# Performance work log

Hardware: AMD Instinct MI355X
Metric: run time of the kernel (lower is better)

The kernel has to match this reference:

```python
import jax, jax.numpy as jnp
import numpy as np

N_QUBITS = 10
N_LAYERS = 2
BATCH = 8192
N_PARAMS = 5 * N_QUBITS * N_LAYERS  # 100
C64 = jnp.complex64

# ---- batched 2x2 gate matrices (theta: (B,)) ----

def _rx(theta):
    h = theta * 0.5
    c = jnp.cos(h).astype(C64)
    s = (-1j * jnp.sin(h).astype(C64))
    return jnp.stack([jnp.stack([c, s], -1), jnp.stack([s, c], -1)], -2)

def _ry(theta):
    h = theta * 0.5
    c = jnp.cos(h).astype(C64)
    s = jnp.sin(h).astype(C64)
    return jnp.stack([jnp.stack([c, -s], -1), jnp.stack([s, c], -1)], -2)

def _rz(theta):
    h = theta.astype(jnp.float32) * 0.5
    e0 = jnp.exp(-1j * h.astype(C64))
    e1 = jnp.exp(1j * h.astype(C64))
    z = jnp.zeros_like(e0)
    return jnp.stack([jnp.stack([e0, z], -1), jnp.stack([z, e1], -1)], -2)

# psi layout: (B, 2, 2, ..., 2); axis 1+w corresponds to wire w (PennyLane order: wire 0 = MSB)

def _apply_1q(psi, mat, w):
    psi = jnp.moveaxis(psi, 1 + w, -1)
    sh = psi.shape
    out = jnp.einsum('bij,bkj->bki', mat, psi.reshape(sh[0], -1, 2))
    return jnp.moveaxis(out.reshape(sh), -1, 1 + w)

def _apply_crx(psi, theta, ctrl, tgt):
    psi = jnp.moveaxis(psi, [1 + ctrl, 1 + tgt], [-2, -1])
    sh = psi.shape
    p = psi.reshape(sh[0], -1, 2, 2)  # axes: (batch, rest, ctrl, tgt)
    h = theta * 0.5
    c = jnp.cos(h)[:, None].astype(C64)
    s = (-1j * jnp.sin(h)[:, None].astype(C64))
    a0 = p[..., 1, 0]
    a1 = p[..., 1, 1]
    p1 = jnp.stack([c * a0 + s * a1, s * a0 + c * a1], -1)
    p = jnp.stack([p[..., 0, :], p1], -2)
    return jnp.moveaxis(p.reshape(sh), [-2, -1], [1 + ctrl, 1 + tgt])

def _init_state(angles):
    B = angles.shape[0]
    psi = jnp.zeros((B, 2 ** N_QUBITS), C64).at[:, 0].set(1.0)
    psi = psi.reshape((B,) + (2,) * N_QUBITS)
    for i in range(N_QUBITS):  # RY input embedding
        psi = _apply_1q(psi, _ry(angles[:, i]), i)
    return psi

def _delta_layer(psi, params, dt, off):
    for i in range(N_QUBITS):
        psi = _apply_1q(psi, _rx(params[:, off] * dt), i)
        psi = _apply_1q(psi, _ry(params[:, off + 1] * dt), i)
        psi = _apply_1q(psi, _rz(params[:, off + 2] * dt), i)
        off += 3
    for i in range(N_QUBITS):
        psi = _apply_crx(psi, params[:, off], i, (i + 1) % N_QUBITS); off += 1
    for i in range(N_QUBITS - 1, -1, -1):
        psi = _apply_crx(psi, params[:, off], i, (i - 1) % N_QUBITS); off += 1
    return psi, off

def _backward_layer(psi, params, dt, off):
    for i in range(N_QUBITS - 1, -1, -1):
        psi = _apply_1q(psi, _rx(params[:, off] * dt), i)
        psi = _apply_1q(psi, _ry(params[:, off + 1] * dt), i)
        psi = _apply_1q(psi, _rz(params[:, off + 2] * dt), i)
        off += 3
    for i in range(N_QUBITS - 1, -1, -1):
        psi = _apply_crx(psi, params[:, off], i, (i - 1) % N_QUBITS); off += 1
    for i in range(N_QUBITS):
        psi = _apply_crx(psi, params[:, off], i, (i + 1) % N_QUBITS); off += 1
    return psi, off

def _unified_layer(psi, params, off):
    for i in range(N_QUBITS):
        psi = _apply_1q(psi, _rx(params[:, off]), i)
        psi = _apply_1q(psi, _ry(params[:, off + 1]), i)
        psi = _apply_1q(psi, _rz(params[:, off + 2]), i)
        off += 3
    for i in range(N_QUBITS):
        psi = _apply_crx(psi, params[:, off], i, (i + 1) % N_QUBITS); off += 1
    for i in range(N_QUBITS - 1, -1, -1):
        psi = _apply_crx(psi, params[:, off], i, (i - 1) % N_QUBITS); off += 1
    return psi, off

def _forward_circuit(angles, params, dt):
    psi = _init_state(angles); off = 0
    for _ in range(N_LAYERS):
        psi, off = _delta_layer(psi, params, dt, off)
    return psi.reshape(psi.shape[0], -1)

def _backward_circuit(angles, params, dt):
    psi = _init_state(angles); off = 0
    for _ in range(N_LAYERS):
        psi, off = _backward_layer(psi, params, dt, off)
    return psi.reshape(psi.shape[0], -1)

def _diagonal_circuit(angles, params):
    psi = _init_state(angles); off = 0
    for _ in range(N_LAYERS):
        psi, off = _unified_layer(psi, params, off)
    return psi.reshape(psi.shape[0], -1)

def _measure(psi_flat):
    # Pauli X/Y/Z expectations per qubit -> (B, 3*n_qubits), ordered [X..., Y..., Z...]
    B = psi_flat.shape[0]
    t = psi_flat.reshape((B,) + (2,) * N_QUBITS)
    Xs, Ys, Zs = [], [], []
    for w in range(N_QUBITS):
        p = jnp.moveaxis(t, 1 + w, -1).reshape(B, -1, 2)
        cross = jnp.sum(jnp.conj(p[..., 0]) * p[..., 1], axis=1)
        Xs.append(2.0 * cross.real)
        Ys.append(2.0 * cross.imag)
        Zs.append(jnp.sum(jnp.abs(p[..., 0]) ** 2 - jnp.abs(p[..., 1]) ** 2, axis=1))
    return jnp.stack(Xs + Ys + Zs, axis=1)

def setup_inputs() -> dict:
    key = jax.random.key(0)
    k1, k2, k3, k4, k5 = jax.random.split(key, 5)
    init_val = np.float32(1.0 / np.sqrt(3.0))
    return {
        'input_angles': jax.random.normal(k1, (BATCH, N_QUBITS), jnp.float32),
        'forward_params': jax.random.normal(k2, (BATCH, N_PARAMS), jnp.float32),
        'backward_params': jax.random.normal(k3, (BATCH, N_PARAMS), jnp.float32),
        'diagonal_params': jax.random.normal(k4, (BATCH, N_PARAMS), jnp.float32),
        'dt_scale': jax.random.uniform(k5, (BATCH,), jnp.float32),
        'alpha_real': jnp.asarray(init_val), 'alpha_imag': jnp.asarray(0.0, jnp.float32),
        'beta_real': jnp.asarray(init_val), 'beta_imag': jnp.asarray(0.0, jnp.float32),
        'gamma_real': jnp.asarray(init_val), 'gamma_imag': jnp.asarray(0.0, jnp.float32),
    }

def reference(input_angles, forward_params, backward_params, diagonal_params, dt_scale,
              alpha_real, alpha_imag, beta_real, beta_imag, gamma_real, gamma_imag):
    psi1 = _forward_circuit(input_angles, forward_params, dt_scale)
    psi2 = _backward_circuit(input_angles, backward_params, dt_scale)
    psi3 = _diagonal_circuit(input_angles, diagonal_params)
    alpha = jax.lax.complex(alpha_real, alpha_imag).astype(C64)
    beta = jax.lax.complex(beta_real, beta_imag).astype(C64)
    gamma = jax.lax.complex(gamma_real, gamma_imag).astype(C64)
    norm = jnp.sqrt(jnp.abs(alpha) ** 2 + jnp.abs(beta) ** 2 + jnp.abs(gamma) ** 2 + 1e-9).astype(C64)
    psi = (alpha / norm) * psi1 + (beta / norm) * psi2 + (gamma / norm) * psi3
    vnorm = jnp.linalg.norm(psi, axis=-1, keepdims=True) + 1e-9
    psi = psi / vnorm.astype(C64)
    return _measure(psi).astype(jnp.float32)
```

## Files before the change

### kernel.cpp

```cpp
#include <hip/hip_runtime.h>

#define NQ    10
#define NPRM  100
#define NBATCH 8192

using F2 = __attribute__((ext_vector_type(2))) float;

__device__ __forceinline__ F2 mk2(float a, float b) { F2 v; v.x = a; v.y = b; return v; }


template<int LM>
__device__ __forceinline__ float lshf(float v) {
  if constexpr (LM == 1) {
    int r = __builtin_amdgcn_update_dpp(0, __builtin_bit_cast(int, v), 0xB1, 0xF, 0xF, true);
    return __builtin_bit_cast(float, r);
  } else if constexpr (LM == 2) {
    int r = __builtin_amdgcn_update_dpp(0, __builtin_bit_cast(int, v), 0x4E, 0xF, 0xF, true);
    return __builtin_bit_cast(float, r);
  } else if constexpr (LM == 8) {
    int r = __builtin_amdgcn_update_dpp(0, __builtin_bit_cast(int, v), 0x128, 0xF, 0xF, true);
    return __builtin_bit_cast(float, r);
  } else {
    return __shfl_xor(v, LM, 64);
  }
}
template<int LM>
__device__ __forceinline__ F2 lshf2(F2 v) {
  return mk2(lshf<LM>(v.x), lshf<LM>(v.y));
}



template<int P>
__device__ __forceinline__ void g_rx(F2* st, unsigned lane, float c, float s) {
  if constexpr (P < 4) {
    constexpr int m = 1 << P;
#pragma unroll
    for (int r = 0; r < 16; ++r) if (!(r & m)) {
      const int r1 = r | m;
      F2 a0 = st[r], a1 = st[r1];
      st[r]  = mk2(c*a0.x + s*a1.y, c*a0.y - s*a1.x);
      st[r1] = mk2(s*a0.y + c*a1.x, c*a1.y - s*a0.x);
    }
  } else {
    constexpr int lm = 1 << (P - 4);
#pragma unroll
    for (int r = 0; r < 16; ++r) {
      float mx = st[r].x, my = st[r].y;
      float ox = lshf<lm>(mx), oy = lshf<lm>(my);
      st[r] = mk2(c*mx + s*oy, c*my - s*ox);
    }
  }
}

template<int P>
__device__ __forceinline__ void g_u(F2* st, unsigned lane, F2 u00, F2 u01) {
  if constexpr (P < 4) {
    constexpr int m = 1 << P;
#pragma unroll
    for (int r = 0; r < 16; ++r) if (!(r & m)) {
      const int r1 = r | m;
      F2 a0 = st[r], a1 = st[r1];
      st[r]  = mk2(u00.x*a0.x - u00.y*a0.y + u01.x*a1.x - u01.y*a1.y,
                   u00.x*a0.y + u00.y*a0.x + u01.x*a1.y + u01.y*a1.x);
      st[r1] = mk2(-u01.x*a0.x - u01.y*a0.y + u00.x*a1.x + u00.y*a1.y,
                   -u01.x*a0.y + u01.y*a0.x + u00.x*a1.y - u00.y*a1.x);
    }
  } else {
    constexpr int lm = 1 << (P - 4);
    const bool hi = (lane & lm) != 0;
    const float vax = u00.x,               vay = hi ? -u00.y : u00.y;
    const float vbx = hi ? -u01.x : u01.x, vby = u01.y;
#pragma unroll
    for (int r = 0; r < 16; ++r) {
      float mx = st[r].x, my = st[r].y;
      float ox = lshf<lm>(mx), oy = lshf<lm>(my);
      st[r] = mk2(vax*mx - vay*my + vbx*ox - vby*oy,
                  vax*my + vay*mx + vbx*oy + vby*ox);
    }
  }
}

template<int TB, int CB>
__device__ __forceinline__ void g_crx(F2* st, unsigned lane, float c, float s) {
  if constexpr (CB >= 4) {
    const bool act = (lane >> (CB - 4)) & 1u;
    const float ce = act ? c : 1.0f;
    const float se = act ? s : 0.0f;
    g_rx<TB>(st, lane, ce, se);
  } else {
    constexpr int cm = 1 << CB;
    if constexpr (TB < 4) {
#pragma unroll
      for (int r = 0; r < 16; ++r) if ((r & cm) && !(r & (1 << TB))) {
        const int r1 = r | (1 << TB);
        F2 a0 = st[r], a1 = st[r1];
        st[r]  = mk2(c*a0.x + s*a1.y, c*a0.y - s*a1.x);
        st[r1] = mk2(s*a0.y + c*a1.x, c*a1.y - s*a0.x);
      }
    } else {
      constexpr int lm = 1 << (TB - 4);
#pragma unroll
      for (int r = 0; r < 16; ++r) if (r & cm) {
        float mx = st[r].x, my = st[r].y;
        float ox = lshf<lm>(mx), oy = lshf<lm>(my);
        st[r] = mk2(c*mx + s*oy, c*my - s*ox);
      }
    }
  }
}

__device__ __forceinline__ void g_u_w(F2* st, unsigned lane, int w, F2 u00, F2 u01) {
  switch (w) {
    case 0: g_u<9>(st,lane,u00,u01); break;
    case 1: g_u<8>(st,lane,u00,u01); break;
    case 2: g_u<7>(st,lane,u00,u01); break;
    case 3: g_u<6>(st,lane,u00,u01); break;
    case 4: g_u<5>(st,lane,u00,u01); break;
    case 5: g_u<4>(st,lane,u00,u01); break;
    case 6: g_u<3>(st,lane,u00,u01); break;
    case 7: g_u<2>(st,lane,u00,u01); break;
    case 8: g_u<1>(st,lane,u00,u01); break;
    case 9: g_u<0>(st,lane,u00,u01); break;
  }
}

#define CRX_CASE(CW,TW) case (CW)*10+(TW): g_crx<9-(TW), 9-(CW)>(st,lane,c,s); break;
__device__ __forceinline__ void crx_w(F2* st, unsigned lane, int cw, int tw, float c, float s) {
  switch (cw * 10 + tw) {
    CRX_CASE(0,1) CRX_CASE(1,2) CRX_CASE(2,3) CRX_CASE(3,4) CRX_CASE(4,5)
    CRX_CASE(5,6) CRX_CASE(6,7) CRX_CASE(7,8) CRX_CASE(8,9) CRX_CASE(9,0)
    CRX_CASE(1,0) CRX_CASE(2,1) CRX_CASE(3,2) CRX_CASE(4,3) CRX_CASE(5,4)
    CRX_CASE(6,5) CRX_CASE(7,6) CRX_CASE(8,7) CRX_CASE(9,8) CRX_CASE(0,9)
  }
}

__device__ __forceinline__ void make_u(float ax, float ay, float az, F2& u00, F2& u01) {
  float ca, sa, cb, sb, cg, sg;
  __sincosf(ax*0.5f, &sa, &ca);
  __sincosf(ay*0.5f, &sb, &cb);
  __sincosf(az*0.5f, &sg, &cg);
  const float m00x =  cb*ca, m00y =  sb*sa;
  const float m01x = -sb*ca, m01y = -cb*sa;
  u00 = mk2(m00x*cg + m00y*sg, m00y*cg - m00x*sg);
  u01 = mk2(m01x*cg + m01y*sg, m01y*cg - m01x*sg);
}

__device__ __forceinline__ void layer_bwd(F2* st, unsigned lane, const float* P, float dt, int& off) {
#pragma unroll
  for (int i = NQ-1; i >= 0; --i) {
    F2 u00, u01;
    make_u(P[off]*dt, P[off+1]*dt, P[off+2]*dt, u00, u01);
    g_u_w(st, lane, i, u00, u01);
    off += 3;
  }
#pragma unroll
  for (int i = NQ-1; i >= 0; --i) {
    float s, c; __sincosf(P[off]*0.5f, &s, &c);
    crx_w(st, lane, i, (i+NQ-1)%NQ, c, s); ++off;
  }
#pragma unroll
  for (int i = 0; i < NQ; ++i) {
    float s, c; __sincosf(P[off]*0.5f, &s, &c);
    crx_w(st, lane, i, (i+1)%NQ, c, s); ++off;
  }
}

__device__ __forceinline__ void init_state(F2* st, unsigned lane, const float* ang) {
  float cw[NQ], sw[NQ];
#pragma unroll
  for (int w = 0; w < NQ; ++w) __sincosf(ang[w]*0.5f, &sw[w], &cw[w]);
  float L = 1.0f;
#pragma unroll
  for (int q = 0; q < 6; ++q)
    L *= ((lane >> q) & 1u) ? sw[5-q] : cw[5-q];
#pragma unroll
  for (int r = 0; r < 16; ++r) {
    float R = L;
#pragma unroll
    for (int p = 0; p < 4; ++p)
      R *= ((r >> p) & 1) ? sw[9-p] : cw[9-p];
    st[r] = mk2(R, 0.0f);
  }
}


struct UU { F2 x00, y00, x01, y01; };

template<int P>
__device__ __forceinline__ void g_u2(F2* sR, F2* sI, unsigned lane, UU u) {
  if constexpr (P < 4) {
    constexpr int m = 1 << P;
#pragma unroll
    for (int r = 0; r < 16; ++r) if (!(r & m)) {
      const int r1 = r | m;
      F2 R0 = sR[r], I0 = sI[r], R1 = sR[r1], I1 = sI[r1];
      sR[r]  = u.x00*R0 - u.y00*I0 + u.x01*R1 - u.y01*I1;
      sI[r]  = u.x00*I0 + u.y00*R0 + u.x01*I1 + u.y01*R1;
      sR[r1] = u.x00*R1 + u.y00*I1 - u.x01*R0 - u.y01*I0;
      sI[r1] = u.x00*I1 - u.y00*R1 - u.x01*I0 + u.y01*R0;
    }
  } else {
    constexpr int lm = 1 << (P - 4);
    const bool hi = (lane & lm) != 0;
    const F2 vay = mk2(hi ? -u.y00.x : u.y00.x, hi ? -u.y00.y : u.y00.y);
    const F2 vbx = mk2(hi ? -u.x01.x : u.x01.x, hi ? -u.x01.y : u.x01.y);
#pragma unroll
    for (int r = 0; r < 16; ++r) {
      F2 R = sR[r], I = sI[r];
      F2 oR = lshf2<lm>(R), oI = lshf2<lm>(I);
      sR[r] = u.x00*R - vay*I + vbx*oR - u.y01*oI;
      sI[r] = u.x00*I + vay*R + vbx*oI + u.y01*oR;
    }
  }
}

template<int P>
__device__ __forceinline__ void g_rx2(F2* sR, F2* sI, unsigned lane, F2 C, F2 S) {
  if constexpr (P < 4) {
    constexpr int m = 1 << P;
#pragma unroll
    for (int r = 0; r < 16; ++r) if (!(r & m)) {
      const int r1 = r | m;
      F2 R0 = sR[r], I0 = sI[r], R1 = sR[r1], I1 = sI[r1];
      sR[r]  = C*R0 + S*I1;
      sI[r]  = C*I0 - S*R1;
      sR[r1] = C*R1 + S*I0;
      sI[r1] = C*I1 - S*R0;
    }
  } else {
    constexpr int lm = 1 << (P - 4);
#pragma unroll
    for (int r = 0; r < 16; ++r) {
      F2 R = sR[r], I = sI[r];
      F2 oR = lshf2<lm>(R), oI = lshf2<lm>(I);
      sR[r] = C*R + S*oI;
      sI[r] = C*I - S*oR;
    }
  }
}

template<int TB, int CB>
__device__ __forceinline__ void g_crx2(F2* sR, F2* sI, unsigned lane, F2 C, F2 S) {
  if constexpr (CB >= 4) {
    const bool act = (lane >> (CB - 4)) & 1u;
    const F2 Ce = mk2(act ? C.x : 1.0f, act ? C.y : 1.0f);
    const F2 Se = mk2(act ? S.x : 0.0f, act ? S.y : 0.0f);
    g_rx2<TB>(sR, sI, lane, Ce, Se);
  } else {
    constexpr int cm = 1 << CB;
    if constexpr (TB < 4) {
#pragma unroll
      for (int r = 0; r < 16; ++r) if ((r & cm) && !(r & (1 << TB))) {
        const int r1 = r | (1 << TB);
        F2 R0 = sR[r], I0 = sI[r], R1 = sR[r1], I1 = sI[r1];
        sR[r]  = C*R0 + S*I1;
        sI[r]  = C*I0 - S*R1;
        sR[r1] = C*R1 + S*I0;
        sI[r1] = C*I1 - S*R0;
      }
    } else {
      constexpr int lm = 1 << (TB - 4);
#pragma unroll
      for (int r = 0; r < 16; ++r) if (r & cm) {
        F2 R = sR[r], I = sI[r];
        F2 oR = lshf2<lm>(R), oI = lshf2<lm>(I);
        sR[r] = C*R + S*oI;
        sI[r] = C*I - S*oR;
      }
    }
  }
}

__device__ __forceinline__ void g_u2_w(F2* sR, F2* sI, unsigned lane, int w, UU u) {
  switch (w) {
    case 0: g_u2<9>(sR,sI,lane,u); break;
    case 1: g_u2<8>(sR,sI,lane,u); break;
    case 2: g_u2<7>(sR,sI,lane,u); break;
    case 3: g_u2<6>(sR,sI,lane,u); break;
    case 4: g_u2<5>(sR,sI,lane,u); break;
    case 5: g_u2<4>(sR,sI,lane,u); break;
    case 6: g_u2<3>(sR,sI,lane,u); break;
    case 7: g_u2<2>(sR,sI,lane,u); break;
    case 8: g_u2<1>(sR,sI,lane,u); break;
    case 9: g_u2<0>(sR,sI,lane,u); break;
  }
}

#define CRX2_CASE(CW,TW) case (CW)*10+(TW): g_crx2<9-(TW), 9-(CW)>(sR,sI,lane,C,S); break;
__device__ __forceinline__ void crx2_w(F2* sR, F2* sI, unsigned lane, int cw, int tw, F2 C, F2 S) {
  switch (cw * 10 + tw) {
    CRX2_CASE(0,1) CRX2_CASE(1,2) CRX2_CASE(2,3) CRX2_CASE(3,4) CRX2_CASE(4,5)
    CRX2_CASE(5,6) CRX2_CASE(6,7) CRX2_CASE(7,8) CRX2_CASE(8,9) CRX2_CASE(9,0)
    CRX2_CASE(1,0) CRX2_CASE(2,1) CRX2_CASE(3,2) CRX2_CASE(4,3) CRX2_CASE(5,4)
    CRX2_CASE(6,5) CRX2_CASE(7,6) CRX2_CASE(8,7) CRX2_CASE(9,8) CRX2_CASE(0,9)
  }
}

__device__ __forceinline__ void layer_fwd2(F2* sR, F2* sI, unsigned lane,
                                           const float* Pf, const float* Pd, float dt, int& off) {
#pragma unroll
  for (int i = 0; i < NQ; ++i) {
    F2 u00F, u01F, u00D, u01D;
    make_u(Pf[off]*dt, Pf[off+1]*dt, Pf[off+2]*dt, u00F, u01F);
    make_u(Pd[off],    Pd[off+1],    Pd[off+2],    u00D, u01D);
    UU u;
    u.x00 = mk2(u00F.x, u00D.x); u.y00 = mk2(u00F.y, u00D.y);
    u.x01 = mk2(u01F.x, u01D.x); u.y01 = mk2(u01F.y, u01D.y);
    g_u2_w(sR, sI, lane, i, u);
    off += 3;
  }
#pragma unroll
  for (int i = 0; i < NQ; ++i) {
    float sF, cF, sD, cD;
    __sincosf(Pf[off]*0.5f, &sF, &cF);
    __sincosf(Pd[off]*0.5f, &sD, &cD);
    crx2_w(sR, sI, lane, i, (i+1)%NQ, mk2(cF,cD), mk2(sF,sD)); ++off;
  }
#pragma unroll
  for (int i = NQ-1; i >= 0; --i) {
    float sF, cF, sD, cD;
    __sincosf(Pf[off]*0.5f, &sF, &cF);
    __sincosf(Pd[off]*0.5f, &sD, &cD);
    crx2_w(sR, sI, lane, i, (i+NQ-1)%NQ, mk2(cF,cD), mk2(sF,sD)); ++off;
  }
}

__device__ __forceinline__ void init_state2(F2* sR, F2* sI, unsigned lane, const float* ang) {
  float cw[NQ], sw[NQ];
#pragma unroll
  for (int w = 0; w < NQ; ++w) __sincosf(ang[w]*0.5f, &sw[w], &cw[w]);
  float L = 1.0f;
#pragma unroll
  for (int q = 0; q < 6; ++q)
    L *= ((lane >> q) & 1u) ? sw[5-q] : cw[5-q];
#pragma unroll
  for (int r = 0; r < 16; ++r) {
    float R = L;
#pragma unroll
    for (int p = 0; p < 4; ++p)
      R *= ((r >> p) & 1) ? sw[9-p] : cw[9-p];
    sR[r] = mk2(R, R);
    sI[r] = mk2(0.0f, 0.0f);
  }
}


template<int P>
__device__ __forceinline__ void meas(const F2* st, unsigned lane, float& X, float& Y, float& Z) {
  float cr = 0.f, ci = 0.f, z = 0.f;
  if constexpr (P < 4) {
    constexpr int m = 1 << P;
#pragma unroll
    for (int r = 0; r < 16; ++r) if (!(r & m)) {
      const int r1 = r | m;
      F2 a0 = st[r], a1 = st[r1];
      cr += a0.x*a1.x + a0.y*a1.y;
      ci += a0.x*a1.y - a0.y*a1.x;
      z  += (a0.x*a0.x + a0.y*a0.y) - (a1.x*a1.x + a1.y*a1.y);
    }
    cr *= 2.f; ci *= 2.f;
  } else {
    constexpr int lm = 1 << (P - 4);
    const bool hi = (lane & lm) != 0;
#pragma unroll
    for (int r = 0; r < 16; ++r) {
      float mx = st[r].x, my = st[r].y;
      float ox = lshf<lm>(mx), oy = lshf<lm>(my);
      float a0x = hi ? ox : mx, a0y = hi ? oy : my;
      float a1x = hi ? mx : ox, a1y = hi ? my : oy;
      cr += a0x*a1x + a0y*a1y;
      ci += a0x*a1y - a0y*a1x;
      float p2 = mx*mx + my*my;
      z += hi ? -p2 : p2;
    }
  }
  X = cr; Y = ci; Z = z;
}

__device__ __forceinline__ float wred(float v) {
  v += lshf<1>(v);
  v += lshf<2>(v);
  v += lshf<4>(v);
  v += lshf<8>(v);
  v += lshf<16>(v);
  v += lshf<32>(v);
  return v;
}


__global__ void __launch_bounds__(256) qsim_kernel(
    const float* __restrict__ angles, const float* __restrict__ fwdP,
    const float* __restrict__ bwdP,   const float* __restrict__ diagP,
    const float* __restrict__ dts,
    const float* __restrict__ ar, const float* __restrict__ ai,
    const float* __restrict__ br, const float* __restrict__ bi,
    const float* __restrict__ gr, const float* __restrict__ gi,
    float* __restrict__ out)
{
  const int tid = blockIdx.x * blockDim.x + threadIdx.x;
  const int b = tid >> 6;
  if (b >= NBATCH) return;
  const unsigned lane = threadIdx.x & 63u;
  const int bu = __builtin_amdgcn_readfirstlane(b);

  const float* ang = angles + bu * NQ;
  const float dt = dts[bu];

  const float arv = ar[0], aiv = ai[0], brv = br[0], biv = bi[0], grv = gr[0], giv = gi[0];
  const float nrm = sqrtf(arv*arv + aiv*aiv + brv*brv + biv*biv + grv*grv + giv*giv + 1e-9f);
  const F2 cA = mk2(arv/nrm, aiv/nrm), cB = mk2(brv/nrm, biv/nrm), cG = mk2(grv/nrm, giv/nrm);

  F2 sR[16], sI[16];
  init_state2(sR, sI, lane, ang);
  { int off = 0;
    const float* Pf = fwdP  + bu*NPRM;
    const float* Pd = diagP + bu*NPRM;
#pragma unroll
    for (int l = 0; l < 2; ++l) layer_fwd2(sR, sI, lane, Pf, Pd, dt, off); }

  F2 stc[16];
#pragma unroll
  for (int r = 0; r < 16; ++r) {
    stc[r] = mk2(cA.x*sR[r].x - cA.y*sI[r].x + cG.x*sR[r].y - cG.y*sI[r].y,
                 cA.x*sI[r].x + cA.y*sR[r].x + cG.x*sI[r].y + cG.y*sR[r].y);
  }

  F2 st[16];
  init_state(st, lane, ang);
  { int off = 0; const float* P = bwdP + bu*NPRM;
#pragma unroll
    for (int l = 0; l < 2; ++l) layer_bwd(st, lane, P, dt, off); }
#pragma unroll
  for (int r = 0; r < 16; ++r) {
    stc[r] = mk2(stc[r].x + cB.x*st[r].x - cB.y*st[r].y,
                 stc[r].y + cB.x*st[r].y + cB.y*st[r].x);
  }

  float n2 = 0.f;
#pragma unroll
  for (int r = 0; r < 16; ++r) n2 += stc[r].x*stc[r].x + stc[r].y*stc[r].y;
  n2 = wred(n2);
  const float inv = 1.0f / (sqrtf(n2) + 1e-9f);
#pragma unroll
  for (int r = 0; r < 16; ++r) { stc[r] = mk2(stc[r].x*inv, stc[r].y*inv); }

  float* o = out + b * 30;
#pragma unroll
  for (int w = 0; w < NQ; ++w) {
    float X, Y, Z;
    switch (w) {
      case 0: meas<9>(stc, lane, X, Y, Z); break;
      case 1: meas<8>(stc, lane, X, Y, Z); break;
      case 2: meas<7>(stc, lane, X, Y, Z); break;
      case 3: meas<6>(stc, lane, X, Y, Z); break;
      case 4: meas<5>(stc, lane, X, Y, Z); break;
      case 5: meas<4>(stc, lane, X, Y, Z); break;
      case 6: meas<3>(stc, lane, X, Y, Z); break;
      case 7: meas<2>(stc, lane, X, Y, Z); break;
      case 8: meas<1>(stc, lane, X, Y, Z); break;
      default: meas<0>(stc, lane, X, Y, Z); break;
    }
    X = wred(X); Y = wred(Y); Z = wred(Z);
    if (lane == 0) { o[w] = X; o[10 + w] = Y; o[20 + w] = Z; }
  }
}

extern "C" void kernel_launch(void* const* d_in, const int* in_sizes, int n_in,
                              void* d_out, int out_size, void* d_ws, size_t ws_size,
                              hipStream_t stream) {
  const float* angles = (const float*)d_in[0];
  const float* fwdP   = (const float*)d_in[1];
  const float* bwdP   = (const float*)d_in[2];
  const float* diagP  = (const float*)d_in[3];
  const float* dts    = (const float*)d_in[4];
  const float* ar     = (const float*)d_in[5];
  const float* ai     = (const float*)d_in[6];
  const float* br     = (const float*)d_in[7];
  const float* bi     = (const float*)d_in[8];
  const float* gr     = (const float*)d_in[9];
  const float* gi     = (const float*)d_in[10];
  float* out = (float*)d_out;

  const int threads = 256;
  const int blocks  = NBATCH / (threads / 64);
  qsim_kernel<<<blocks, threads, 0, stream>>>(
      angles, fwdP, bwdP, diagP, dts, ar, ai, br, bi, gr, gi, out);
}
```

Baseline: 289.2 us.

## Split three circuits across waves, pack two batch items per wave

```diff
diff --git a/kernel.cpp b/kernel.cpp
--- a/kernel.cpp
+++ b/kernel.cpp
@@ -29,160 +29,6 @@
   return mk2(lshf<LM>(v.x), lshf<LM>(v.y));
 }
 
-
-
-template<int P>
-__device__ __forceinline__ void g_rx(F2* st, unsigned lane, float c, float s) {
-  if constexpr (P < 4) {
-    constexpr int m = 1 << P;
-#pragma unroll
-    for (int r = 0; r < 16; ++r) if (!(r & m)) {
-      const int r1 = r | m;
-      F2 a0 = st[r], a1 = st[r1];
-      st[r]  = mk2(c*a0.x + s*a1.y, c*a0.y - s*a1.x);
-      st[r1] = mk2(s*a0.y + c*a1.x, c*a1.y - s*a0.x);
-    }
-  } else {
-    constexpr int lm = 1 << (P - 4);
-#pragma unroll
-    for (int r = 0; r < 16; ++r) {
-      float mx = st[r].x, my = st[r].y;
-      float ox = lshf<lm>(mx), oy = lshf<lm>(my);
-      st[r] = mk2(c*mx + s*oy, c*my - s*ox);
-    }
-  }
-}
-
-template<int P>
-__device__ __forceinline__ void g_u(F2* st, unsigned lane, F2 u00, F2 u01) {
-  if constexpr (P < 4) {
-    constexpr int m = 1 << P;
-#pragma unroll
-    for (int r = 0; r < 16; ++r) if (!(r & m)) {
-      const int r1 = r | m;
-      F2 a0 = st[r], a1 = st[r1];
-      st[r]  = mk2(u00.x*a0.x - u00.y*a0.y + u01.x*a1.x - u01.y*a1.y,
-                   u00.x*a0.y + u00.y*a0.x + u01.x*a1.y + u01.y*a1.x);
-      st[r1] = mk2(-u01.x*a0.x - u01.y*a0.y + u00.x*a1.x + u00.y*a1.y,
-                   -u01.x*a0.y + u01.y*a0.x + u00.x*a1.y - u00.y*a1.x);
-    }
-  } else {
-    constexpr int lm = 1 << (P - 4);
-    const bool hi = (lane & lm) != 0;
-    const float vax = u00.x,               vay = hi ? -u00.y : u00.y;
-    const float vbx = hi ? -u01.x : u01.x, vby = u01.y;
-#pragma unroll
-    for (int r = 0; r < 16; ++r) {
-      float mx = st[r].x, my = st[r].y;
-      float ox = lshf<lm>(mx), oy = lshf<lm>(my);
-      st[r] = mk2(vax*mx - vay*my + vbx*ox - vby*oy,
-                  vax*my + vay*mx + vbx*oy + vby*ox);
-    }
-  }
-}
-
-template<int TB, int CB>
-__device__ __forceinline__ void g_crx(F2* st, unsigned lane, float c, float s) {
-  if constexpr (CB >= 4) {
-    const bool act = (lane >> (CB - 4)) & 1u;
-    const float ce = act ? c : 1.0f;
-    const float se = act ? s : 0.0f;
-    g_rx<TB>(st, lane, ce, se);
-  } else {
-    constexpr int cm = 1 << CB;
-    if constexpr (TB < 4) {
-#pragma unroll
-      for (int r = 0; r < 16; ++r) if ((r & cm) && !(r & (1 << TB))) {
-        const int r1 = r | (1 << TB);
-        F2 a0 = st[r], a1 = st[r1];
-        st[r]  = mk2(c*a0.x + s*a1.y, c*a0.y - s*a1.x);
-        st[r1] = mk2(s*a0.y + c*a1.x, c*a1.y - s*a0.x);
-      }
-    } else {
-      constexpr int lm = 1 << (TB - 4);
-#pragma unroll
-      for (int r = 0; r < 16; ++r) if (r & cm) {
-        float mx = st[r].x, my = st[r].y;
-        float ox = lshf<lm>(mx), oy = lshf<lm>(my);
-        st[r] = mk2(c*mx + s*oy, c*my - s*ox);
-      }
-    }
-  }
-}
-
-__device__ __forceinline__ void g_u_w(F2* st, unsigned lane, int w, F2 u00, F2 u01) {
-  switch (w) {
-    case 0: g_u<9>(st,lane,u00,u01); break;
-    case 1: g_u<8>(st,lane,u00,u01); break;
-    case 2: g_u<7>(st,lane,u00,u01); break;
-    case 3: g_u<6>(st,lane,u00,u01); break;
-    case 4: g_u<5>(st,lane,u00,u01); break;
-    case 5: g_u<4>(st,lane,u00,u01); break;
-    case 6: g_u<3>(st,lane,u00,u01); break;
-    case 7: g_u<2>(st,lane,u00,u01); break;
-    case 8: g_u<1>(st,lane,u00,u01); break;
-    case 9: g_u<0>(st,lane,u00,u01); break;
-  }
-}
-
-#define CRX_CASE(CW,TW) case (CW)*10+(TW): g_crx<9-(TW), 9-(CW)>(st,lane,c,s); break;
-__device__ __forceinline__ void crx_w(F2* st, unsigned lane, int cw, int tw, float c, float s) {
-  switch (cw * 10 + tw) {
-    CRX_CASE(0,1) CRX_CASE(1,2) CRX_CASE(2,3) CRX_CASE(3,4) CRX_CASE(4,5)
-    CRX_CASE(5,6) CRX_CASE(6,7) CRX_CASE(7,8) CRX_CASE(8,9) CRX_CASE(9,0)
-    CRX_CASE(1,0) CRX_CASE(2,1) CRX_CASE(3,2) CRX_CASE(4,3) CRX_CASE(5,4)
-    CRX_CASE(6,5) CRX_CASE(7,6) CRX_CASE(8,7) CRX_CASE(9,8) CRX_CASE(0,9)
-  }
-}
-
-__device__ __forceinline__ void make_u(float ax, float ay, float az, F2& u00, F2& u01) {
-  float ca, sa, cb, sb, cg, sg;
-  __sincosf(ax*0.5f, &sa, &ca);
-  __sincosf(ay*0.5f, &sb, &cb);
-  __sincosf(az*0.5f, &sg, &cg);
-  const float m00x =  cb*ca, m00y =  sb*sa;
-  const float m01x = -sb*ca, m01y = -cb*sa;
-  u00 = mk2(m00x*cg + m00y*sg, m00y*cg - m00x*sg);
-  u01 = mk2(m01x*cg + m01y*sg, m01y*cg - m01x*sg);
-}
-
-__device__ __forceinline__ void layer_bwd(F2* st, unsigned lane, const float* P, float dt, int& off) {
-#pragma unroll
-  for (int i = NQ-1; i >= 0; --i) {
-    F2 u00, u01;
-    make_u(P[off]*dt, P[off+1]*dt, P[off+2]*dt, u00, u01);
-    g_u_w(st, lane, i, u00, u01);
-    off += 3;
-  }
-#pragma unroll
-  for (int i = NQ-1; i >= 0; --i) {
-    float s, c; __sincosf(P[off]*0.5f, &s, &c);
-    crx_w(st, lane, i, (i+NQ-1)%NQ, c, s); ++off;
-  }
-#pragma unroll
-  for (int i = 0; i < NQ; ++i) {
-    float s, c; __sincosf(P[off]*0.5f, &s, &c);
-    crx_w(st, lane, i, (i+1)%NQ, c, s); ++off;
-  }
-}
-
-__device__ __forceinline__ void init_state(F2* st, unsigned lane, const float* ang) {
-  float cw[NQ], sw[NQ];
-#pragma unroll
-  for (int w = 0; w < NQ; ++w) __sincosf(ang[w]*0.5f, &sw[w], &cw[w]);
-  float L = 1.0f;
-#pragma unroll
-  for (int q = 0; q < 6; ++q)
-    L *= ((lane >> q) & 1u) ? sw[5-q] : cw[5-q];
-#pragma unroll
-  for (int r = 0; r < 16; ++r) {
-    float R = L;
-#pragma unroll
-    for (int p = 0; p < 4; ++p)
-      R *= ((r >> p) & 1) ? sw[9-p] : cw[9-p];
-    st[r] = mk2(R, 0.0f);
-  }
-}
 
 
 struct UU { F2 x00, y00, x01, y01; };
@@ -297,99 +143,147 @@
   }
 }
 
+__device__ __forceinline__ void make_u(float ax, float ay, float az, F2& u00, F2& u01) {
+  float ca, sa, cb, sb, cg, sg;
+  __sincosf(ax*0.5f, &sa, &ca);
+  __sincosf(ay*0.5f, &sb, &cb);
+  __sincosf(az*0.5f, &sg, &cg);
+  const float m00x =  cb*ca, m00y =  sb*sa;
+  const float m01x = -sb*ca, m01y = -cb*sa;
+  u00 = mk2(m00x*cg + m00y*sg, m00y*cg - m00x*sg);
+  u01 = mk2(m01x*cg + m01y*sg, m01y*cg - m01x*sg);
+}
+
+__device__ __forceinline__ UU pack_u(const float* P0, const float* P1, float dt0, float dt1, int off) {
+  F2 u00a, u01a, u00b, u01b;
+  make_u(P0[off]*dt0, P0[off+1]*dt0, P0[off+2]*dt0, u00a, u01a);
+  make_u(P1[off]*dt1, P1[off+1]*dt1, P1[off+2]*dt1, u00b, u01b);
+  UU u;
+  u.x00 = mk2(u00a.x, u00b.x); u.y00 = mk2(u00a.y, u00b.y);
+  u.x01 = mk2(u01a.x, u01b.x); u.y01 = mk2(u01a.y, u01b.y);
+  return u;
+}
+
+__device__ __forceinline__ void pack_cs(const float* P0, const float* P1, int off, F2& C, F2& S) {
+  float s0, c0, s1, c1;
+  __sincosf(P0[off]*0.5f, &s0, &c0);
+  __sincosf(P1[off]*0.5f, &s1, &c1);
+  C = mk2(c0, c1); S = mk2(s0, s1);
+}
+
 __device__ __forceinline__ void layer_fwd2(F2* sR, F2* sI, unsigned lane,
-                                           const float* Pf, const float* Pd, float dt, int& off) {
+                                           const float* P0, const float* P1,
+                                           float dt0, float dt1, int& off) {
 #pragma unroll
   for (int i = 0; i < NQ; ++i) {
-    F2 u00F, u01F, u00D, u01D;
-    make_u(Pf[off]*dt, Pf[off+1]*dt, Pf[off+2]*dt, u00F, u01F);
-    make_u(Pd[off],    Pd[off+1],    Pd[off+2],    u00D, u01D);
-    UU u;
-    u.x00 = mk2(u00F.x, u00D.x); u.y00 = mk2(u00F.y, u00D.y);
-    u.x01 = mk2(u01F.x, u01D.x); u.y01 = mk2(u01F.y, u01D.y);
-    g_u2_w(sR, sI, lane, i, u);
+    g_u2_w(sR, sI, lane, i, pack_u(P0, P1, dt0, dt1, off));
     off += 3;
   }
 #pragma unroll
   for (int i = 0; i < NQ; ++i) {
-    float sF, cF, sD, cD;
-    __sincosf(Pf[off]*0.5f, &sF, &cF);
-    __sincosf(Pd[off]*0.5f, &sD, &cD);
-    crx2_w(sR, sI, lane, i, (i+1)%NQ, mk2(cF,cD), mk2(sF,sD)); ++off;
+    F2 C, S; pack_cs(P0, P1, off, C, S);
+    crx2_w(sR, sI, lane, i, (i+1)%NQ, C, S); ++off;
   }
 #pragma unroll
   for (int i = NQ-1; i >= 0; --i) {
-    float sF, cF, sD, cD;
-    __sincosf(Pf[off]*0.5f, &sF, &cF);
-    __sincosf(Pd[off]*0.5f, &sD, &cD);
-    crx2_w(sR, sI, lane, i, (i+NQ-1)%NQ, mk2(cF,cD), mk2(sF,sD)); ++off;
-  }
-}
-
-__device__ __forceinline__ void init_state2(F2* sR, F2* sI, unsigned lane, const float* ang) {
-  float cw[NQ], sw[NQ];
-#pragma unroll
-  for (int w = 0; w < NQ; ++w) __sincosf(ang[w]*0.5f, &sw[w], &cw[w]);
-  float L = 1.0f;
-#pragma unroll
-  for (int q = 0; q < 6; ++q)
-    L *= ((lane >> q) & 1u) ? sw[5-q] : cw[5-q];
+    F2 C, S; pack_cs(P0, P1, off, C, S);
+    crx2_w(sR, sI, lane, i, (i+NQ-1)%NQ, C, S); ++off;
+  }
+}
+
+__device__ __forceinline__ void layer_bwd2(F2* sR, F2* sI, unsigned lane,
+                                           const float* P0, const float* P1,
+                                           float dt0, float dt1, int& off) {
+#pragma unroll
+  for (int i = NQ-1; i >= 0; --i) {
+    g_u2_w(sR, sI, lane, i, pack_u(P0, P1, dt0, dt1, off));
+    off += 3;
+  }
+#pragma unroll
+  for (int i = NQ-1; i >= 0; --i) {
+    F2 C, S; pack_cs(P0, P1, off, C, S);
+    crx2_w(sR, sI, lane, i, (i+NQ-1)%NQ, C, S); ++off;
+  }
+#pragma unroll
+  for (int i = 0; i < NQ; ++i) {
+    F2 C, S; pack_cs(P0, P1, off, C, S);
+    crx2_w(sR, sI, lane, i, (i+1)%NQ, C, S); ++off;
+  }
+}
+
+__device__ __forceinline__ void init_state2e(F2* sR, F2* sI, unsigned lane,
+                                             const float* ang0, const float* ang1) {
+  float cw0[NQ], sw0[NQ], cw1[NQ], sw1[NQ];
+#pragma unroll
+  for (int w = 0; w < NQ; ++w) {
+    __sincosf(ang0[w]*0.5f, &sw0[w], &cw0[w]);
+    __sincosf(ang1[w]*0.5f, &sw1[w], &cw1[w]);
+  }
+  F2 L = mk2(1.0f, 1.0f);
+#pragma unroll
+  for (int q = 0; q < 6; ++q) {
+    const int w = 5-q;
+    L *= ((lane >> q) & 1u) ? mk2(sw0[w], sw1[w]) : mk2(cw0[w], cw1[w]);
+  }
 #pragma unroll
   for (int r = 0; r < 16; ++r) {
-    float R = L;
-#pragma unroll
-    for (int p = 0; p < 4; ++p)
-      R *= ((r >> p) & 1) ? sw[9-p] : cw[9-p];
-    sR[r] = mk2(R, R);
+    F2 R = L;
+#pragma unroll
+    for (int p = 0; p < 4; ++p) {
+      const int w = 9-p;
+      R *= ((r >> p) & 1) ? mk2(sw0[w], sw1[w]) : mk2(cw0[w], cw1[w]);
+    }
+    sR[r] = R;
     sI[r] = mk2(0.0f, 0.0f);
   }
 }
 
 
 template<int P>
-__device__ __forceinline__ void meas(const F2* st, unsigned lane, float& X, float& Y, float& Z) {
-  float cr = 0.f, ci = 0.f, z = 0.f;
+__device__ __forceinline__ void meas2(const F2* sRe, const F2* sIm, unsigned lane,
+                                      F2& X, F2& Y, F2& Z) {
+  F2 cr = mk2(0,0), ci = mk2(0,0), z = mk2(0,0);
   if constexpr (P < 4) {
     constexpr int m = 1 << P;
 #pragma unroll
     for (int r = 0; r < 16; ++r) if (!(r & m)) {
       const int r1 = r | m;
-      F2 a0 = st[r], a1 = st[r1];
-      cr += a0.x*a1.x + a0.y*a1.y;
-      ci += a0.x*a1.y - a0.y*a1.x;
-      z  += (a0.x*a0.x + a0.y*a0.y) - (a1.x*a1.x + a1.y*a1.y);
-    }
-    cr *= 2.f; ci *= 2.f;
+      F2 aR = sRe[r], aI = sIm[r], bR = sRe[r1], bI = sIm[r1];
+      cr += aR*bR + aI*bI;
+      ci += aR*bI - aI*bR;
+      z  += (aR*aR + aI*aI) - (bR*bR + bI*bI);
+    }
+    cr = cr + cr; ci = ci + ci;
   } else {
     constexpr int lm = 1 << (P - 4);
     const bool hi = (lane & lm) != 0;
 #pragma unroll
     for (int r = 0; r < 16; ++r) {
-      float mx = st[r].x, my = st[r].y;
-      float ox = lshf<lm>(mx), oy = lshf<lm>(my);
-      float a0x = hi ? ox : mx, a0y = hi ? oy : my;
-      float a1x = hi ? mx : ox, a1y = hi ? my : oy;
-      cr += a0x*a1x + a0y*a1y;
-      ci += a0x*a1y - a0y*a1x;
-      float p2 = mx*mx + my*my;
+      F2 mR = sRe[r], mI = sIm[r];
+      F2 oR = lshf2<lm>(mR), oI = lshf2<lm>(mI);
+      F2 a0R = hi ? oR : mR, a0I = hi ? oI : mI;
+      F2 a1R = hi ? mR : oR, a1I = hi ? mI : oI;
+      cr += a0R*a1R + a0I*a1I;
+      ci += a0R*a1I - a0I*a1R;
+      F2 p2 = mR*mR + mI*mI;
       z += hi ? -p2 : p2;
     }
   }
   X = cr; Y = ci; Z = z;
 }
 
-__device__ __forceinline__ float wred(float v) {
-  v += lshf<1>(v);
-  v += lshf<2>(v);
-  v += lshf<4>(v);
-  v += lshf<8>(v);
-  v += lshf<16>(v);
-  v += lshf<32>(v);
+__device__ __forceinline__ F2 wred2(F2 v) {
+  v += lshf2<1>(v);
+  v += lshf2<2>(v);
+  v += lshf2<4>(v);
+  v += lshf2<8>(v);
+  v += lshf2<16>(v);
+  v += lshf2<32>(v);
   return v;
 }
 
 
-__global__ void __launch_bounds__(256) qsim_kernel(
+__global__ void __launch_bounds__(192, 2) qsim_kernel(
     const float* __restrict__ angles, const float* __restrict__ fwdP,
     const float* __restrict__ bwdP,   const float* __restrict__ diagP,
     const float* __restrict__ dts,
@@ -398,71 +292,96 @@
     const float* __restrict__ gr, const float* __restrict__ gi,
     float* __restrict__ out)
 {
-  const int tid = blockIdx.x * blockDim.x + threadIdx.x;
-  const int b = tid >> 6;
-  if (b >= NBATCH) return;
+  __shared__ F2 ldsR[2][16][64];
+  __shared__ F2 ldsI[2][16][64];
+
+  const int wave = threadIdx.x >> 6;
   const unsigned lane = threadIdx.x & 63u;
-  const int bu = __builtin_amdgcn_readfirstlane(b);
-
-  const float* ang = angles + bu * NQ;
-  const float dt = dts[bu];
+  const int b0 = blockIdx.x * 2;
+  const int b1 = b0 + 1;
+
+  const float* ang0 = angles + b0 * NQ;
+  const float* ang1 = angles + b1 * NQ;
+  const float dt0 = dts[b0], dt1 = dts[b1];
 
   const float arv = ar[0], aiv = ai[0], brv = br[0], biv = bi[0], grv = gr[0], giv = gi[0];
   const float nrm = sqrtf(arv*arv + aiv*aiv + brv*brv + biv*biv + grv*grv + giv*giv + 1e-9f);
-  const F2 cA = mk2(arv/nrm, aiv/nrm), cB = mk2(brv/nrm, biv/nrm), cG = mk2(grv/nrm, giv/nrm);
+  const float cAx = arv/nrm, cAy = aiv/nrm;
+  const float cBx = brv/nrm, cBy = biv/nrm;
+  const float cGx = grv/nrm, cGy = giv/nrm;
 
   F2 sR[16], sI[16];
-  init_state2(sR, sI, lane, ang);
-  { int off = 0;
-    const float* Pf = fwdP  + bu*NPRM;
-    const float* Pd = diagP + bu*NPRM;
-#pragma unroll
-    for (int l = 0; l < 2; ++l) layer_fwd2(sR, sI, lane, Pf, Pd, dt, off); }
-
-  F2 stc[16];
+  init_state2e(sR, sI, lane, ang0, ang1);
+
+  if (wave == 0) {
+    int off = 0;
+    const float* P0 = fwdP + b0*NPRM;
+    const float* P1 = fwdP + b1*NPRM;
+#pragma unroll
+    for (int l = 0; l < 2; ++l) layer_fwd2(sR, sI, lane, P0, P1, dt0, dt1, off);
+  } else if (wave == 1) {
+    int off = 0;
+    const float* P0 = bwdP + b0*NPRM;
+    const float* P1 = bwdP + b1*NPRM;
+#pragma unroll
+    for (int l = 0; l < 2; ++l) layer_bwd2(sR, sI, lane, P0, P1, dt0, dt1, off);
+  } else {
+    int off = 0;
+    const float* P0 = diagP + b0*NPRM;
+    const float* P1 = diagP + b1*NPRM;
+#pragma unroll
+    for (int l = 0; l < 2; ++l) layer_fwd2(sR, sI, lane, P0, P1, 1.0f, 1.0f, off);
+  }
+
+  if (wave != 0) {
+    const float wx = (wave == 1) ? cBx : cGx;
+    const float wy = (wave == 1) ? cBy : cGy;
+#pragma unroll
+    for (int r = 0; r < 16; ++r) {
+      ldsR[wave-1][r][lane] = wx*sR[r] - wy*sI[r];
+      ldsI[wave-1][r][lane] = wx*sI[r] + wy*sR[r];
+    }
+  }
+  __syncthreads();
+  if (wave != 0) return;
+
 #pragma unroll
   for (int r = 0; r < 16; ++r) {
-    stc[r] = mk2(cA.x*sR[r].x - cA.y*sI[r].x + cG.x*sR[r].y - cG.y*sI[r].y,
-                 cA.x*sI[r].x + cA.y*sR[r].x + cG.x*sI[r].y + cG.y*sR[r].y);
-  }
-
-  F2 st[16];
-  init_state(st, lane, ang);
-  { int off = 0; const float* P = bwdP + bu*NPRM;
-#pragma unroll
-    for (int l = 0; l < 2; ++l) layer_bwd(st, lane, P, dt, off); }
-#pragma unroll
-  for (int r = 0; r < 16; ++r) {
-    stc[r] = mk2(stc[r].x + cB.x*st[r].x - cB.y*st[r].y,
-                 stc[r].y + cB.x*st[r].y + cB.y*st[r].x);
-  }
-
-  float n2 = 0.f;
-#pragma unroll
-  for (int r = 0; r < 16; ++r) n2 += stc[r].x*stc[r].x + stc[r].y*stc[r].y;
-  n2 = wred(n2);
-  const float inv = 1.0f / (sqrtf(n2) + 1e-9f);
-#pragma unroll
-  for (int r = 0; r < 16; ++r) { stc[r] = mk2(stc[r].x*inv, stc[r].y*inv); }
-
-  float* o = out + b * 30;
+    F2 nR = cAx*sR[r] - cAy*sI[r] + ldsR[0][r][lane] + ldsR[1][r][lane];
+    F2 nI = cAx*sI[r] + cAy*sR[r] + ldsI[0][r][lane] + ldsI[1][r][lane];
+    sR[r] = nR; sI[r] = nI;
+  }
+
+  F2 n2 = mk2(0.0f, 0.0f);
+#pragma unroll
+  for (int r = 0; r < 16; ++r) n2 += sR[r]*sR[r] + sI[r]*sI[r];
+  n2 = wred2(n2);
+  const F2 inv = mk2(1.0f/(sqrtf(n2.x)+1e-9f), 1.0f/(sqrtf(n2.y)+1e-9f));
+#pragma unroll
+  for (int r = 0; r < 16; ++r) { sR[r] *= inv; sI[r] *= inv; }
+
+  float* o0 = out + b0 * 30;
+  float* o1 = out + b1 * 30;
 #pragma unroll
   for (int w = 0; w < NQ; ++w) {
-    float X, Y, Z;
+    F2 X, Y, Z;
     switch (w) {
-      case 0: meas<9>(stc, lane, X, Y, Z); break;
-      case 1: meas<8>(stc, lane, X, Y, Z); break;
-      case 2: meas<7>(stc, lane, X, Y, Z); break;
-      case 3: meas<6>(stc, lane, X, Y, Z); break;
-      case 4: meas<5>(stc, lane, X, Y, Z); break;
-      case 5: meas<4>(stc, lane, X, Y, Z); break;
-      case 6: meas<3>(stc, lane, X, Y, Z); break;
-      case 7: meas<2>(stc, lane, X, Y, Z); break;
-      case 8: meas<1>(stc, lane, X, Y, Z); break;
-      default: meas<0>(stc, lane, X, Y, Z); break;
-    }
-    X = wred(X); Y = wred(Y); Z = wred(Z);
-    if (lane == 0) { o[w] = X; o[10 + w] = Y; o[20 + w] = Z; }
+      case 0: meas2<9>(sR, sI, lane, X, Y, Z); break;
+      case 1: meas2<8>(sR, sI, lane, X, Y, Z); break;
+      case 2: meas2<7>(sR, sI, lane, X, Y, Z); break;
+      case 3: meas2<6>(sR, sI, lane, X, Y, Z); break;
+      case 4: meas2<5>(sR, sI, lane, X, Y, Z); break;
+      case 5: meas2<4>(sR, sI, lane, X, Y, Z); break;
+      case 6: meas2<3>(sR, sI, lane, X, Y, Z); break;
+      case 7: meas2<2>(sR, sI, lane, X, Y, Z); break;
+      case 8: meas2<1>(sR, sI, lane, X, Y, Z); break;
+      default: meas2<0>(sR, sI, lane, X, Y, Z); break;
+    }
+    X = wred2(X); Y = wred2(Y); Z = wred2(Z);
+    if (lane == 0) {
+      o0[w] = X.x; o0[10 + w] = Y.x; o0[20 + w] = Z.x;
+      o1[w] = X.y; o1[10 + w] = Y.y; o1[20 + w] = Z.y;
+    }
   }
 }
 
@@ -482,8 +401,6 @@
   const float* gi     = (const float*)d_in[10];
   float* out = (float*)d_out;
 
-  const int threads = 256;
-  const int blocks  = NBATCH / (threads / 64);
-  qsim_kernel<<<blocks, threads, 0, stream>>>(
+  qsim_kernel<<<NBATCH/2, 192, 0, stream>>>(
       angles, fwdP, bwdP, diagP, dts, ar, ai, br, bi, gr, gi, out);
 }
```

Measured after the change: 289.6 us. Within noise of the previous version (+0.1%).
